# Kernel optimization log

Hardware: AMD Instinct MI355X
Metric: run time of the kernel (lower is better)

The kernel has to match this reference:

```python
import jax, jax.numpy as jnp
import numpy as np

LAMBDA = 25.0
MU = 25.0
NU = 1.0
ALPHA = 0.25
EPS = 1e-4
NUM_MATCHES = (20, 4)


def _cdist(x, y):
    # x: (B, L1, C), y: (B, L2, C) -> (B, L1, L2) euclidean distances
    x2 = jnp.sum(x * x, axis=-1)[..., :, None]
    y2 = jnp.sum(y * y, axis=-1)[..., None, :]
    d2 = x2 + y2 - 2.0 * jnp.einsum('blc,bmc->blm', x, y)
    return jnp.sqrt(jnp.maximum(d2, 0.0))


def _nearest_neighbors(input_maps, candidate_maps, distances, num_matches):
    # For each input location, its nearest candidate; then keep the
    # num_matches input locations with smallest NN distance, in original order.
    nn_dist = jnp.min(distances, axis=-1)    # (B, L1)
    nn_idx = jnp.argmin(distances, axis=-1)  # (B, L1)
    _, sel = jax.lax.top_k(-nn_dist, num_matches)  # (B, M) smallest distances
    sel = jnp.sort(sel, axis=1)  # restore original ordering of positions
    filtered_input = jnp.take_along_axis(input_maps, sel[..., None], axis=1)
    nn_sel = jnp.take_along_axis(nn_idx, sel, axis=1)
    filtered_candidate = jnp.take_along_axis(candidate_maps, nn_sel[..., None], axis=1)
    return filtered_input, filtered_candidate


def _mse(a, b):
    return jnp.mean((a - b) ** 2)


def _vicreg_loss(z_a, z_b):
    inv_loss = _mse(z_a, z_b)

    def var_loss(z):
        std = jnp.sqrt(jnp.var(z, axis=0, ddof=1) + EPS)
        return jnp.mean(jax.nn.relu(1.0 - std))

    def cov_loss(z):
        n, d = z.shape
        zc = z - jnp.mean(z, axis=0)
        cov = (zc.T @ zc) / (n - 1)
        off = cov - jnp.diag(jnp.diag(cov))
        return jnp.sum(off ** 2) / d

    v = 0.5 * (var_loss(z_a) + var_loss(z_b))
    c = cov_loss(z_a) + cov_loss(z_b)
    return LAMBDA * inv_loss + MU * v + NU * c


def _local_loss(z_global, z_local, grid_global, grid_local):
    B = z_global.shape[0]
    zg = z_global.reshape(B, -1, z_global.shape[-1])   # (B, Lg, C)
    zl = z_local.reshape(B, -1, z_local.shape[-1])     # (B, Ll, C)

    inv_loss = 0.0
    # feature-space NN
    gf, gn = _nearest_neighbors(zg, zl, _cdist(zg, zl), NUM_MATCHES[0])
    lf, ln = _nearest_neighbors(zl, zg, _cdist(zl, zg), NUM_MATCHES[1])
    inv_loss = inv_loss + (_mse(gf, gn) / 2 + _mse(lf, ln) / 2)

    # grid-space NN (distances from grids, gather from feature maps)
    gg = grid_global.reshape(B, -1, 2)
    gl = grid_local.reshape(B, -1, 2)
    gf, gn = _nearest_neighbors(zg, zl, _cdist(gg, gl), NUM_MATCHES[0])
    lf, ln = _nearest_neighbors(zl, zg, _cdist(gl, gg), NUM_MATCHES[1])
    inv_loss = inv_loss + (_mse(gf, gn) / 2 + _mse(lf, ln) / 2)

    return LAMBDA * inv_loss


def setup_inputs() -> dict:
    key = jax.random.key(0)
    ks = jax.random.split(key, 6)
    B, D, C = 32, 8192, 512
    return {
        'z_global': jax.random.normal(ks[0], (B, D), jnp.float32),
        'z_local': jax.random.normal(ks[1], (B, D), jnp.float32),
        'z_global_local_features': jax.random.normal(ks[2], (B, 24, 24, C), jnp.float32),
        'z_local_local_features': jax.random.normal(ks[3], (B, 16, 16, C), jnp.float32),
        'grid_global': jax.random.uniform(ks[4], (B, 24, 24, 2), jnp.float32),
        'grid_local': jax.random.uniform(ks[5], (B, 16, 16, 2), jnp.float32),
    }


def reference(z_global, z_local, z_global_local_features, z_local_local_features, grid_global, grid_local):
    global_loss = _vicreg_loss(z_global, z_local)
    local_loss = _local_loss(z_global_local_features, z_local_local_features, grid_global, grid_local)
    return ALPHA * global_loss + (1.0 - ALPHA) * local_loss
```

## Files before the change

### kernel.cpp

```cpp
#include <hip/hip_runtime.h>
#include <hip/hip_bf16.h>

#define BATCH 32
#define DZ    8192
#define LG    576
#define LL    256
#define CH    512

#define OFF_S      0
#define OFF_BSUM   8192
#define OFF_SELSUM 9472
#define OFF_CNT    10496
#define OFF_RNP    10560
#define OFF_CNP    305472
#define WS_NEED    895296

typedef __attribute__((ext_vector_type(8))) short bf16x8;
typedef __attribute__((ext_vector_type(4))) float f32x4;

__device__ __forceinline__ unsigned short f2bf(float x) {
  union { __hip_bfloat16 h; unsigned short u; } cv;
  cv.h = __float2bfloat16(x);
  return cv.u;
}

__device__ __forceinline__ uint4 pack8(float4 lo, float4 hi) {
  union { unsigned short h[8]; uint4 u; } pk;
  pk.h[0] = f2bf(lo.x); pk.h[1] = f2bf(lo.y); pk.h[2] = f2bf(lo.z); pk.h[3] = f2bf(lo.w);
  pk.h[4] = f2bf(hi.x); pk.h[5] = f2bf(hi.y); pk.h[6] = f2bf(hi.z); pk.h[7] = f2bf(hi.w);
  return pk.u;
}

__device__ __forceinline__ float dot4(float4 v) {
  return v.x * v.x + v.y * v.y + v.z * v.z + v.w * v.w;
}

struct SelSmem {
  unsigned long long keys[LG];
  unsigned int nnm[LG];
  float cxy[2 * LG];
  unsigned int plist[40];
  unsigned int cnt;
  float fred[4];
};

template <int V>
__device__ __forceinline__ void sel_case(
    SelSmem& sm, int b,
    const float* __restrict__ zgf, const float* __restrict__ zlf,
    const float* __restrict__ gg, const float* __restrict__ gl,
    const unsigned long long* __restrict__ rowNNp,
    const unsigned long long* __restrict__ colNNp,
    double* __restrict__ selsum) {
  constexpr bool GDIR = (V == 0 || V == 2);
  constexpr int L1 = GDIR ? LG : LL;
  constexpr int L2 = GDIR ? LL : LG;
  constexpr int M  = GDIR ? 20 : 4;
  constexpr int NR = (L1 + 255) / 256;
  const float* fin  = GDIR ? zgf + (size_t)b * LG * CH : zlf + (size_t)b * LL * CH;
  const float* fcan = GDIR ? zlf + (size_t)b * LL * CH : zgf + (size_t)b * LG * CH;
  int tid = threadIdx.x, lane = tid & 63, wv = tid >> 6;
  if (tid == 0) sm.cnt = 0;

  if constexpr (V < 2) {
    constexpr int P = (V == 0) ? 2 : 9;
    const unsigned long long* src =
        (V == 0) ? rowNNp + (size_t)b * LG * 2 : colNNp + (size_t)b * LL * 9;
    #pragma unroll
    for (int s = 0; s < NR; ++s) {
      int l = tid + s * 256;
      if (l < L1) {
        const unsigned long long* q = src + (size_t)l * P;
        unsigned long long p = q[0];
        #pragma unroll
        for (int u = 1; u < P; ++u) { unsigned long long t2 = q[u]; p = t2 < p ? t2 : p; }
        sm.keys[l] = (p & 0xFFFFFFFF00000000ull) | (unsigned)l;
        sm.nnm[l] = (unsigned)(p & 0xFFFFFFFFu);
      }
    }
  } else {
    const float* gin  = (V == 2) ? gg + (size_t)b * LG * 2 : gl + (size_t)b * LL * 2;
    const float* gcan = (V == 2) ? gl + (size_t)b * LL * 2 : gg + (size_t)b * LG * 2;
    #pragma unroll
    for (int s = 0; s < (2 * L2 + 255) / 256; ++s) {
      int i = tid + s * 256;
      if (i < 2 * L2) sm.cxy[i] = gcan[i];
    }
    __syncthreads();
    float x[NR], y[NR], bd[NR];
    unsigned bi[NR];
    #pragma unroll
    for (int s = 0; s < NR; ++s) {
      int l = tid + s * 256;
      x[s] = (l < L1) ? gin[2 * l] : 0.f;
      y[s] = (l < L1) ? gin[2 * l + 1] : 0.f;
      bd[s] = 3.4e38f; bi[s] = 0;
    }
    const float2* c2 = (const float2*)sm.cxy;
    for (int m2 = 0; m2 < L2; m2 += 8) {
      float2 cc[8];
      #pragma unroll
      for (int u = 0; u < 8; ++u) cc[u] = c2[m2 + u];
      #pragma unroll
      for (int u = 0; u < 8; ++u)
        #pragma unroll
        for (int s = 0; s < NR; ++s) {
          float dx = x[s] - cc[u].x, dy = y[s] - cc[u].y;
          float d2 = dx * dx + dy * dy;
          if (d2 < bd[s]) { bd[s] = d2; bi[s] = (unsigned)(m2 + u); }
        }
    }
    #pragma unroll
    for (int s = 0; s < NR; ++s) {
      int l = tid + s * 256;
      if (l < L1) {
        sm.keys[l] = ((unsigned long long)__float_as_uint(bd[s]) << 32) | (unsigned)l;
        sm.nnm[l] = bi[s];
      }
    }
  }
  __syncthreads();

  unsigned long long myk[NR];
  int rk[NR];
  #pragma unroll
  for (int s = 0; s < NR; ++s) {
    int l = tid + s * 256;
    myk[s] = (l < L1) ? sm.keys[l] : ~0ull;
    rk[s] = 0;
  }
  for (int j = 0; j < L1; j += 8) {
    unsigned long long kk[8];
    #pragma unroll
    for (int u = 0; u < 8; ++u) kk[u] = sm.keys[j + u];
    #pragma unroll
    for (int u = 0; u < 8; ++u)
      #pragma unroll
      for (int s = 0; s < NR; ++s) rk[s] += (kk[u] < myk[s]) ? 1 : 0;
  }
  #pragma unroll
  for (int s = 0; s < NR; ++s) {
    int l = tid + s * 256;
    if (l < L1 && rk[s] < M) {
      unsigned slot = atomicAdd(&sm.cnt, 1u);
      sm.plist[2 * slot] = (unsigned)l;
      sm.plist[2 * slot + 1] = sm.nnm[l];
    }
  }
  __syncthreads();

  float part = 0.f;
  #pragma unroll
  for (int rr = 0; rr < M / 4; ++rr) {
    int r = wv + rr * 4;
    const float4* a4 = (const float4*)(fin + (size_t)sm.plist[2 * r] * CH);
    const float4* c4 = (const float4*)(fcan + (size_t)sm.plist[2 * r + 1] * CH);
    float4 xa = a4[lane * 2], xb = a4[lane * 2 + 1];
    float4 ya = c4[lane * 2], yb = c4[lane * 2 + 1];
    float d0 = xa.x - ya.x, d1 = xa.y - ya.y, d2 = xa.z - ya.z, d3 = xa.w - ya.w;
    float d4 = xb.x - yb.x, d5 = xb.y - yb.y, d6 = xb.z - yb.z, d7 = xb.w - yb.w;
    part += d0 * d0 + d1 * d1 + d2 * d2 + d3 * d3 +
            d4 * d4 + d5 * d5 + d6 * d6 + d7 * d7;
  }
  for (int s = 32; s; s >>= 1) part += __shfl_down(part, s);
  if (lane == 0) sm.fred[wv] = part;
  __syncthreads();
  if (tid == 0)
    selsum[V * 32 + b] = (double)(sm.fred[0] + sm.fred[1] + sm.fred[2] + sm.fred[3]);
}

__global__ __launch_bounds__(256) void k_megaA(
    const float* __restrict__ za, const float* __restrict__ zb,
    const float* __restrict__ zgf, const float* __restrict__ zlf,
    const float* __restrict__ gg, const float* __restrict__ gl,
    double* __restrict__ bsum, float* __restrict__ S,
    unsigned long long* __restrict__ rowNNp, unsigned long long* __restrict__ colNNp,
    double* __restrict__ selsum, unsigned int* __restrict__ cnt) {
  __shared__ __align__(16) char smem[28416];
  int tid = threadIdx.x, lane = tid & 63, wv = tid >> 6;
  int blk = blockIdx.x;

  if (blk < 64) {
    SelSmem& sm = *reinterpret_cast<SelSmem*>(smem);
    int b2 = blk >> 1;
    if (blk & 1) sel_case<3>(sm, b2, zgf, zlf, gg, gl, rowNNp, colNNp, selsum);
    else         sel_case<2>(sm, b2, zgf, zlf, gg, gl, rowNNp, colNNp, selsum);
    return;
  }

  if (blk < 640) {
    int fblk = blk - 64;
    int fs = (fblk & 7) * 72 + (fblk >> 3);
    int b = fs / 18, rr_ = fs % 18;
    int by = rr_ / 9, bx = rr_ % 9;
    int row0 = bx * 64, col0 = by * 128;

    unsigned short (*As)[72] = (unsigned short(*)[72])smem;
    unsigned short (*Bs)[72] = (unsigned short(*)[72])(smem + 9216);
    float* Asn = (float*)(smem + 27648);
    float* Bsn = (float*)(smem + 27904);

    const int m16 = lane & 15, quad = lane >> 4;
    const int wm = wv >> 1, wn = wv & 1;
    const float* Ag = zgf + ((size_t)(b * LG + row0)) * CH;
    const float* Bg = zlf + ((size_t)(b * LL + col0)) * CH;
    const int sr = tid >> 2, sq = tid & 3;
    const int br = tid >> 1, bq = tid & 1;

    f32x4 acc[2][4] = {};
    float ssA = 0.f, ssB = 0.f;
    float4 a0, a1, a2, a3, b0, b1, b2, b3, b4, b5, b6, b7;

    {
      const float* ap = Ag + (size_t)sr * CH + sq * 16;
      a0 = *(const float4*)(ap);      a1 = *(const float4*)(ap + 4);
      a2 = *(const float4*)(ap + 8);  a3 = *(const float4*)(ap + 12);
      const float* bp = Bg + (size_t)br * CH + bq * 16;
      b0 = *(const float4*)(bp);      b1 = *(const float4*)(bp + 4);
      b2 = *(const float4*)(bp + 8);  b3 = *(const float4*)(bp + 12);
      b4 = *(const float4*)(bp + 32); b5 = *(const float4*)(bp + 36);
      b6 = *(const float4*)(bp + 40); b7 = *(const float4*)(bp + 44);
    }

    #pragma unroll
    for (int t = 0; t < 8; ++t) {
      __syncthreads();
      *(uint4*)&As[sr][sq * 16]      = pack8(a0, a1);
      *(uint4*)&As[sr][sq * 16 + 8]  = pack8(a2, a3);
      *(uint4*)&Bs[br][bq * 16]      = pack8(b0, b1);
      *(uint4*)&Bs[br][bq * 16 + 8]  = pack8(b2, b3);
      *(uint4*)&Bs[br][bq * 16 + 32] = pack8(b4, b5);
      *(uint4*)&Bs[br][bq * 16 + 40] = pack8(b6, b7);
      ssA += dot4(a0) + dot4(a1) + dot4(a2) + dot4(a3);
      ssB += dot4(b0) + dot4(b1) + dot4(b2) + dot4(b3) +
             dot4(b4) + dot4(b5) + dot4(b6) + dot4(b7);
      __syncthreads();
      if (t < 7) {
        int k0 = (t + 1) * 64;
        const float* ap = Ag + (size_t)sr * CH + k0 + sq * 16;
        a0 = *(const float4*)(ap);      a1 = *(const float4*)(ap + 4);
        a2 = *(const float4*)(ap + 8);  a3 = *(const float4*)(ap + 12);
        const float* bp = Bg + (size_t)br * CH + k0 + bq * 16;
        b0 = *(const float4*)(bp);      b1 = *(const float4*)(bp + 4);
        b2 = *(const float4*)(bp + 8);  b3 = *(const float4*)(bp + 12);
        b4 = *(const float4*)(bp + 32); b5 = *(const float4*)(bp + 36);
        b6 = *(const float4*)(bp + 40); b7 = *(const float4*)(bp + 44);
      }
      #pragma unroll
      for (int kk = 0; kk < 64; kk += 32) {
        bf16x8 af0 = *(const bf16x8*)&As[wm * 32 + m16][kk + quad * 8];
        bf16x8 af1 = *(const bf16x8*)&As[wm * 32 + 16 + m16][kk + quad * 8];
        bf16x8 bfv[4];
        #pragma unroll
        for (int j = 0; j < 4; ++j)
          bfv[j] = *(const bf16x8*)&Bs[wn * 64 + j * 16 + m16][kk + quad * 8];
        #pragma unroll
        for (int j = 0; j < 4; ++j) {
          acc[0][j] = __builtin_amdgcn_mfma_f32_16x16x32_bf16(af0, bfv[j], acc[0][j], 0, 0, 0);
          acc[1][j] = __builtin_amdgcn_mfma_f32_16x16x32_bf16(af1, bfv[j], acc[1][j], 0, 0, 0);
        }
      }
    }

    ssA += __shfl_xor(ssA, 1); ssA += __shfl_xor(ssA, 2);
    ssB += __shfl_xor(ssB, 1);
    if (sq == 0) Asn[sr] = ssA;
    if (bq == 0) Bsn[br] = ssB;
    __syncthreads();

    float na[2][4], nb[4];
    #pragma unroll
    for (int i = 0; i < 2; ++i)
      #pragma unroll
      for (int r = 0; r < 4; ++r)
        na[i][r] = Asn[wm * 32 + i * 16 + quad * 4 + r];
    #pragma unroll
    for (int j = 0; j < 4; ++j)
      nb[j] = Bsn[wn * 64 + j * 16 + m16];

    #pragma unroll
    for (int i = 0; i < 2; ++i) {
      #pragma unroll
      for (int r = 0; r < 4; ++r) {
        unsigned long long p = ~0ull;
        #pragma unroll
        for (int j = 0; j < 4; ++j) {
          float d = fmaxf(na[i][r] + nb[j] - 2.f * acc[i][j][r], 0.f);
          unsigned c = (unsigned)(col0 + wn * 64 + j * 16 + m16);
          unsigned long long pj = (((unsigned long long)__float_as_uint(d)) << 32) | c;
          p = pj < p ? pj : p;
        }
        #pragma unroll
        for (int s = 1; s < 16; s <<= 1) {
          unsigned long long q = __shfl_xor(p, s);
          p = q < p ? q : p;
        }
        if (m16 == 0)
          rowNNp[((size_t)b * LG + row0 + wm * 32 + i * 16 + quad * 4 + r) * 2 + by] = p;
      }
    }
    #pragma unroll
    for (int j = 0; j < 4; ++j) {
      unsigned long long p = ~0ull;
      #pragma unroll
      for (int i = 0; i < 2; ++i) {
        #pragma unroll
        for (int r = 0; r < 4; ++r) {
          float d = fmaxf(na[i][r] + nb[j] - 2.f * acc[i][j][r], 0.f);
          unsigned rg = (unsigned)(row0 + wm * 32 + i * 16 + quad * 4 + r);
          unsigned long long pr = (((unsigned long long)__float_as_uint(d)) << 32) | rg;
          p = pr < p ? pr : p;
        }
      }
      unsigned long long q = __shfl_xor(p, 16); p = q < p ? q : p;
      q = __shfl_xor(p, 32); p = q < p ? q : p;
      if (quad == 0)
        colNNp[((size_t)b * LL + col0 + wn * 64 + j * 16 + m16) * 9 + bx] = p;
    }
    return;
  }

  if (blk < 1696) {
    float (*sred)[5] = (float(*)[5])smem;
    int e = blk - 640;
    int zi = e >= 528; if (zi) e -= 528;
    const float* z = zi ? zb : za;
    float* Sz = S + zi * 1024;
    int p = 0, rem = e;
    while (rem >= 32 - p) { rem -= 32 - p; ++p; }
    int q = p + rem;
    const float4* zp = (const float4*)(z + (size_t)p * DZ);
    const float4* zq = (const float4*)(z + (size_t)q * DZ);
    float s = 0.f;
    #pragma unroll
    for (int ii = 0; ii < 8; ++ii) {
      int i = tid + ii * 256;
      float4 a = zp[i], bb = zq[i];
      s += a.x * bb.x + a.y * bb.y + a.z * bb.z + a.w * bb.w;
    }
    for (int off = 32; off; off >>= 1) s += __shfl_down(s, off);
    if (lane == 0) sred[wv][0] = s;
    __syncthreads();
    if (tid == 0) {
      float r = sred[0][0] + sred[1][0] + sred[2][0] + sred[3][0];
      Sz[p * 32 + q] = r;
      if (p != q) Sz[q * 32 + p] = r;
    }
    return;
  }

  {
    float (*sred)[5] = (float(*)[5])smem;
    int blkS = blk - 1696;
    if (blkS == 0 && tid == 0) cnt[0] = 0;
    int i = blkS * 256 + tid;
    float sa = 0.f, qa = 0.f, sb = 0.f, qb = 0.f, si = 0.f;
    #pragma unroll 8
    for (int b = 0; b < BATCH; ++b) {
      float va = za[(size_t)b * DZ + i];
      float vb = zb[(size_t)b * DZ + i];
      sa += va; qa += va * va;
      sb += vb; qb += vb * vb;
      float d = va - vb; si += d * d;
    }
    float ssa = qa - sa * sa * (1.f / 32.f);
    float ssb = qb - sb * sb * (1.f / 32.f);
    float v0 = si;
    float v1 = fmaxf(0.f, 1.f - sqrtf(ssa * (1.f / 31.f) + 1e-4f));
    float v2 = fmaxf(0.f, 1.f - sqrtf(ssb * (1.f / 31.f) + 1e-4f));
    float v3 = ssa * ssa, v4 = ssb * ssb;
    for (int off = 32; off; off >>= 1) {
      v0 += __shfl_down(v0, off); v1 += __shfl_down(v1, off);
      v2 += __shfl_down(v2, off); v3 += __shfl_down(v3, off);
      v4 += __shfl_down(v4, off);
    }
    if (lane == 0) {
      sred[wv][0] = v0; sred[wv][1] = v1; sred[wv][2] = v2;
      sred[wv][3] = v3; sred[wv][4] = v4;
    }
    __syncthreads();
    if (tid < 5)
      bsum[blkS * 5 + tid] =
          (double)(sred[0][tid] + sred[1][tid] + sred[2][tid] + sred[3][tid]);
  }
}

struct TailSmem {
  SelSmem sel;
  float t[2][32];
  double sacc[5];
  double smf[4];
  int isLast;
};

__global__ __launch_bounds__(256) void k_tail(
    const float* __restrict__ zgf, const float* __restrict__ zlf,
    const float* __restrict__ gg, const float* __restrict__ gl,
    const unsigned long long* __restrict__ rowNNp,
    const unsigned long long* __restrict__ colNNp,
    double* __restrict__ selsum, const double* __restrict__ bsum,
    const float* __restrict__ S, unsigned int* __restrict__ doneCnt,
    float* __restrict__ out) {
  __shared__ TailSmem ts;
  int tid = threadIdx.x;
  int b = blockIdx.x >> 1, V = blockIdx.x & 1;
  if (V == 0) sel_case<0>(ts.sel, b, zgf, zlf, gg, gl, rowNNp, colNNp, selsum);
  else        sel_case<1>(ts.sel, b, zgf, zlf, gg, gl, rowNNp, colNNp, selsum);

  if (tid == 0) {
    __threadfence();
    unsigned r = atomicAdd(doneCnt, 1u);
    ts.isLast = (r == 63) ? 1 : 0;
  }
  __syncthreads();
  if (!ts.isLast) return;
  __threadfence();

  if (tid < 32) {
    #pragma unroll
    for (int zi = 0; zi < 2; ++zi) {
      float tp = 0.f;
      for (int bb = 0; bb < 32; ++bb) tp += S[zi * 1024 + tid * 32 + bb];
      ts.t[zi][tid] = tp * (1.f / 32.f);
    }
  }
  if (tid < 5) {
    double s = 0.0;
    for (int blk2 = 0; blk2 < 32; ++blk2) s += bsum[blk2 * 5 + tid];
    ts.sacc[tid] = s;
  }
  if (tid >= 8 && tid < 12) {
    int v = tid - 8;
    double s = 0.0;
    for (int bb = 0; bb < 32; ++bb) s += selsum[v * 32 + bb];
    ts.smf[v] = s;
  }
  __syncthreads();
  if (tid < 64) {
    double total[2];
    #pragma unroll
    for (int zi = 0; zi < 2; ++zi) {
      float u = 0.f;
      for (int bb = 0; bb < 32; ++bb) u += ts.t[zi][bb];
      u *= (1.f / 32.f);
      double s = 0.0;
      for (int e2 = tid; e2 < 1024; e2 += 64) {
        int p = e2 >> 5, q = e2 & 31;
        float G = S[zi * 1024 + e2] - ts.t[zi][p] - ts.t[zi][q] + u;
        s += (double)G * (double)G;
      }
      for (int off = 32; off; off >>= 1) s += __shfl_down(s, off);
      total[zi] = s;
    }
    if (tid == 0) {
      double inv_g = ts.sacc[0] / (32.0 * 8192.0);
      double v = 0.5 * (ts.sacc[1] + ts.sacc[2]) / 8192.0;
      double c = (total[0] - ts.sacc[3] + total[1] - ts.sacc[4]) / (961.0 * 8192.0);
      double gloss = 25.0 * inv_g + 25.0 * v + c;
      double mfg = ts.smf[0] / (32.0 * 20.0 * 512.0);
      double mfl = ts.smf[1] / (32.0 * 4.0 * 512.0);
      double mgg = ts.smf[2] / (32.0 * 20.0 * 512.0);
      double mgl = ts.smf[3] / (32.0 * 4.0 * 512.0);
      double lloss = 25.0 * (0.5 * (mfg + mfl) + 0.5 * (mgg + mgl));
      out[0] = (float)(0.25 * gloss + 0.75 * lloss);
    }
  }
}

extern "C" void kernel_launch(void* const* d_in, const int* in_sizes, int n_in,
                              void* d_out, int out_size, void* d_ws, size_t ws_size,
                              hipStream_t stream) {
  const float* zg  = (const float*)d_in[0];
  const float* zl  = (const float*)d_in[1];
  const float* zgf = (const float*)d_in[2];
  const float* zlf = (const float*)d_in[3];
  const float* gg  = (const float*)d_in[4];
  const float* glo = (const float*)d_in[5];

  char* ws = (char*)d_ws;
  float* S       = (float*)(ws + OFF_S);
  double* bsum   = (double*)(ws + OFF_BSUM);
  double* selsum = (double*)(ws + OFF_SELSUM);
  unsigned int* cnt = (unsigned int*)(ws + OFF_CNT);
  unsigned long long* rowNNp = (unsigned long long*)(ws + OFF_RNP);
  unsigned long long* colNNp = (unsigned long long*)(ws + OFF_CNP);

  k_megaA<<<1728, 256, 0, stream>>>(zg, zl, zgf, zlf, gg, glo,
                                    bsum, S, rowNNp, colNNp, selsum, cnt);
  k_tail<<<64, 256, 0, stream>>>(zgf, zlf, gg, glo, rowNNp, colNNp,
                                 selsum, bsum, S, cnt, (float*)d_out);
}
```

Measured before the change: 138.5 us.

## Double-buffer LDS tiles with K=32 steps in the distance GEMM blocks

The single-buffered K=64 LDS staging in the cdist GEMM section is replaced by two ping-pong LDS buffers with K=32 per stage. Each stage stores the prefetched tile into the other buffer while MFMAs run on the current one, so there is one barrier per stage instead of two per tile. This aims to overlap LDS writes and global loads with matrix work and to cut register pressure from prefetch. The trade-off is more stages and barriers overall, slightly more shared memory, and a row stride of 40 halfwords that may change bank-conflict behaviour.

```diff
diff --git a/kernel.cpp b/kernel.cpp
--- a/kernel.cpp
+++ b/kernel.cpp
@@ -176,7 +176,7 @@
     double* __restrict__ bsum, float* __restrict__ S,
     unsigned long long* __restrict__ rowNNp, unsigned long long* __restrict__ colNNp,
     double* __restrict__ selsum, unsigned int* __restrict__ cnt) {
-  __shared__ __align__(16) char smem[28416];
+  __shared__ __align__(16) char smem[31488];
   int tid = threadIdx.x, lane = tid & 63, wv = tid >> 6;
   int blk = blockIdx.x;
 
@@ -195,10 +195,12 @@
     int by = rr_ / 9, bx = rr_ % 9;
     int row0 = bx * 64, col0 = by * 128;
 
-    unsigned short (*As)[72] = (unsigned short(*)[72])smem;
-    unsigned short (*Bs)[72] = (unsigned short(*)[72])(smem + 9216);
-    float* Asn = (float*)(smem + 27648);
-    float* Bsn = (float*)(smem + 27904);
+    unsigned short (*As0)[40] = (unsigned short(*)[40])smem;
+    unsigned short (*Bs0)[40] = (unsigned short(*)[40])(smem + 5120);
+    unsigned short (*As1)[40] = (unsigned short(*)[40])(smem + 15360);
+    unsigned short (*Bs1)[40] = (unsigned short(*)[40])(smem + 20480);
+    float* Asn = (float*)(smem + 30720);
+    float* Bsn = (float*)(smem + 30976);
 
     const int m16 = lane & 15, quad = lane >> 4;
     const int wm = wv >> 1, wn = wv & 1;
@@ -209,61 +211,81 @@
 
     f32x4 acc[2][4] = {};
     float ssA = 0.f, ssB = 0.f;
-    float4 a0, a1, a2, a3, b0, b1, b2, b3, b4, b5, b6, b7;
-
-    {
-      const float* ap = Ag + (size_t)sr * CH + sq * 16;
-      a0 = *(const float4*)(ap);      a1 = *(const float4*)(ap + 4);
-      a2 = *(const float4*)(ap + 8);  a3 = *(const float4*)(ap + 12);
-      const float* bp = Bg + (size_t)br * CH + bq * 16;
-      b0 = *(const float4*)(bp);      b1 = *(const float4*)(bp + 4);
-      b2 = *(const float4*)(bp + 8);  b3 = *(const float4*)(bp + 12);
-      b4 = *(const float4*)(bp + 32); b5 = *(const float4*)(bp + 36);
-      b6 = *(const float4*)(bp + 40); b7 = *(const float4*)(bp + 44);
-    }
-
-    #pragma unroll
-    for (int t = 0; t < 8; ++t) {
-      __syncthreads();
-      *(uint4*)&As[sr][sq * 16]      = pack8(a0, a1);
-      *(uint4*)&As[sr][sq * 16 + 8]  = pack8(a2, a3);
-      *(uint4*)&Bs[br][bq * 16]      = pack8(b0, b1);
-      *(uint4*)&Bs[br][bq * 16 + 8]  = pack8(b2, b3);
-      *(uint4*)&Bs[br][bq * 16 + 32] = pack8(b4, b5);
-      *(uint4*)&Bs[br][bq * 16 + 40] = pack8(b6, b7);
-      ssA += dot4(a0) + dot4(a1) + dot4(a2) + dot4(a3);
-      ssB += dot4(b0) + dot4(b1) + dot4(b2) + dot4(b3) +
-             dot4(b4) + dot4(b5) + dot4(b6) + dot4(b7);
-      __syncthreads();
-      if (t < 7) {
-        int k0 = (t + 1) * 64;
-        const float* ap = Ag + (size_t)sr * CH + k0 + sq * 16;
-        a0 = *(const float4*)(ap);      a1 = *(const float4*)(ap + 4);
-        a2 = *(const float4*)(ap + 8);  a3 = *(const float4*)(ap + 12);
-        const float* bp = Bg + (size_t)br * CH + k0 + bq * 16;
-        b0 = *(const float4*)(bp);      b1 = *(const float4*)(bp + 4);
-        b2 = *(const float4*)(bp + 8);  b3 = *(const float4*)(bp + 12);
-        b4 = *(const float4*)(bp + 32); b5 = *(const float4*)(bp + 36);
-        b6 = *(const float4*)(bp + 40); b7 = *(const float4*)(bp + 44);
-      }
-      #pragma unroll
-      for (int kk = 0; kk < 64; kk += 32) {
-        bf16x8 af0 = *(const bf16x8*)&As[wm * 32 + m16][kk + quad * 8];
-        bf16x8 af1 = *(const bf16x8*)&As[wm * 32 + 16 + m16][kk + quad * 8];
+    float4 a0, a1, b0, b1, b2, b3;
+
+    const float* apb = Ag + (size_t)sr * CH + sq * 8;
+    const float* bpb = Bg + (size_t)br * CH + bq * 16;
+
+    a0 = *(const float4*)(apb);     a1 = *(const float4*)(apb + 4);
+    b0 = *(const float4*)(bpb);     b1 = *(const float4*)(bpb + 4);
+    b2 = *(const float4*)(bpb + 8); b3 = *(const float4*)(bpb + 12);
+    *(uint4*)&As0[sr][sq * 8]       = pack8(a0, a1);
+    *(uint4*)&Bs0[br][bq * 16]      = pack8(b0, b1);
+    *(uint4*)&Bs0[br][bq * 16 + 8]  = pack8(b2, b3);
+    ssA += dot4(a0) + dot4(a1);
+    ssB += dot4(b0) + dot4(b1) + dot4(b2) + dot4(b3);
+    a0 = *(const float4*)(apb + 32);      a1 = *(const float4*)(apb + 36);
+    b0 = *(const float4*)(bpb + 32);      b1 = *(const float4*)(bpb + 36);
+    b2 = *(const float4*)(bpb + 40);      b3 = *(const float4*)(bpb + 44);
+    __syncthreads();
+
+    #pragma unroll
+    for (int k = 0; k < 8; ++k) {
+      {
+        bf16x8 af0 = *(const bf16x8*)&As0[wm * 32 + m16][quad * 8];
+        bf16x8 af1 = *(const bf16x8*)&As0[wm * 32 + 16 + m16][quad * 8];
         bf16x8 bfv[4];
         #pragma unroll
         for (int j = 0; j < 4; ++j)
-          bfv[j] = *(const bf16x8*)&Bs[wn * 64 + j * 16 + m16][kk + quad * 8];
+          bfv[j] = *(const bf16x8*)&Bs0[wn * 64 + j * 16 + m16][quad * 8];
         #pragma unroll
         for (int j = 0; j < 4; ++j) {
           acc[0][j] = __builtin_amdgcn_mfma_f32_16x16x32_bf16(af0, bfv[j], acc[0][j], 0, 0, 0);
           acc[1][j] = __builtin_amdgcn_mfma_f32_16x16x32_bf16(af1, bfv[j], acc[1][j], 0, 0, 0);
         }
+        *(uint4*)&As1[sr][sq * 8]      = pack8(a0, a1);
+        *(uint4*)&Bs1[br][bq * 16]     = pack8(b0, b1);
+        *(uint4*)&Bs1[br][bq * 16 + 8] = pack8(b2, b3);
+        ssA += dot4(a0) + dot4(a1);
+        ssB += dot4(b0) + dot4(b1) + dot4(b2) + dot4(b3);
+        if (k < 7) {
+          int k0 = (2 * k + 2) * 32;
+          a0 = *(const float4*)(apb + k0);      a1 = *(const float4*)(apb + k0 + 4);
+          b0 = *(const float4*)(bpb + k0);      b1 = *(const float4*)(bpb + k0 + 4);
+          b2 = *(const float4*)(bpb + k0 + 8);  b3 = *(const float4*)(bpb + k0 + 12);
+        }
+        __syncthreads();
+      }
+      {
+        bf16x8 af0 = *(const bf16x8*)&As1[wm * 32 + m16][quad * 8];
+        bf16x8 af1 = *(const bf16x8*)&As1[wm * 32 + 16 + m16][quad * 8];
+        bf16x8 bfv[4];
+        #pragma unroll
+        for (int j = 0; j < 4; ++j)
+          bfv[j] = *(const bf16x8*)&Bs1[wn * 64 + j * 16 + m16][quad * 8];
+        #pragma unroll
+        for (int j = 0; j < 4; ++j) {
+          acc[0][j] = __builtin_amdgcn_mfma_f32_16x16x32_bf16(af0, bfv[j], acc[0][j], 0, 0, 0);
+          acc[1][j] = __builtin_amdgcn_mfma_f32_16x16x32_bf16(af1, bfv[j], acc[1][j], 0, 0, 0);
+        }
+        if (k < 7) {
+          *(uint4*)&As0[sr][sq * 8]      = pack8(a0, a1);
+          *(uint4*)&Bs0[br][bq * 16]     = pack8(b0, b1);
+          *(uint4*)&Bs0[br][bq * 16 + 8] = pack8(b2, b3);
+          ssA += dot4(a0) + dot4(a1);
+          ssB += dot4(b0) + dot4(b1) + dot4(b2) + dot4(b3);
+          int k0 = (2 * k + 3) * 32;
+          a0 = *(const float4*)(apb + k0);      a1 = *(const float4*)(apb + k0 + 4);
+          b0 = *(const float4*)(bpb + k0);      b1 = *(const float4*)(bpb + k0 + 4);
+          b2 = *(const float4*)(bpb + k0 + 8);  b3 = *(const float4*)(bpb + k0 + 12);
+          __syncthreads();
+        }
       }
     }
 
     ssA += __shfl_xor(ssA, 1); ssA += __shfl_xor(ssA, 2);
     ssB += __shfl_xor(ssB, 1);
+    __syncthreads();
     if (sq == 0) Asn[sr] = ssA;
     if (bq == 0) Bsn[br] = ssB;
     __syncthreads();
```

Result: no change. 137.9 us, median of 2 (-0.4%).
